# Kernel tuning notes

Measured on AMD Instinct MI355X. Metric: run time of the kernel, lower is better.

Reference implementation:

```python
import jax, jax.numpy as jnp
import numpy as np

N = 20000      # nodes
E = 320000     # directed edges (before self loops)
IN_DIM = 384
D = 256        # hidden_dim
H = 4          # heads
C = D // H     # per-head channels = 64
L = 3          # layers
NEG_SLOPE = 0.2
LN_EPS = 1e-5


def setup_inputs() -> dict:
    key = jax.random.key(0)
    ks = jax.random.split(key, 8)
    return {
        "x": jax.random.normal(ks[0], (N, IN_DIM), jnp.float32),
        "edge_index": jax.random.randint(ks[1], (2, E), 0, N),
        "w_in": jax.random.normal(ks[2], (IN_DIM, D), jnp.float32) * 0.05,
        "b_in": jnp.zeros((D,), jnp.float32),
        "wl": jax.random.normal(ks[3], (L, D, D), jnp.float32) * 0.05,
        "wr": jax.random.normal(ks[4], (L, D, D), jnp.float32) * 0.05,
        "att": jax.random.normal(ks[5], (L, H, C), jnp.float32) * 0.05,
        "bias": jnp.zeros((L, D), jnp.float32),
        "ln_g": jnp.ones((L, D), jnp.float32),
        "ln_b": jnp.zeros((L, D), jnp.float32),
    }


def _layernorm(h, g, b):
    mu = jnp.mean(h, axis=-1, keepdims=True)
    var = jnp.mean(jnp.square(h - mu), axis=-1, keepdims=True)
    return (h - mu) * jax.lax.rsqrt(var + LN_EPS) * g + b


def _gatv2(h, src, dst, Wl, Wr, a, b):
    # PyG GATv2Conv, concat=True, eval mode (no dropout), self-loops already in src/dst.
    xl = (h @ Wl).reshape(N, H, C)   # source transform (lin_l)
    xr = (h @ Wr).reshape(N, H, C)   # target transform (lin_r)
    x_j = xl[src]                    # [E', H, C] gathered source messages
    e = jnp.einsum('ehc,hc->eh', jax.nn.leaky_relu(x_j + xr[dst], NEG_SLOPE), a)
    # segment softmax over edges grouped by destination node
    m = jax.ops.segment_max(e, dst, num_segments=N)
    e = jnp.exp(e - m[dst])
    s = jax.ops.segment_sum(e, dst, num_segments=N)
    alpha = e / (s[dst] + 1e-16)     # [E', H]
    out = jax.ops.segment_sum(x_j * alpha[:, :, None], dst, num_segments=N)
    return out.reshape(N, D) + b


def reference(x, edge_index, w_in, b_in, wl, wr, att, bias, ln_g, ln_b):
    loops = jnp.arange(N, dtype=edge_index.dtype)
    src = jnp.concatenate([edge_index[0], loops])
    dst = jnp.concatenate([edge_index[1], loops])
    h = x @ w_in + b_in
    for l in range(L):
        h_new = _layernorm(_gatv2(h, src, dst, wl[l], wr[l], att[l], bias[l]),
                           ln_g[l], ln_b[l])
        h = h + h_new  # shapes always match since concat output == hidden_dim
    norm = jnp.linalg.norm(h, axis=-1, keepdims=True)
    return h / jnp.maximum(norm, 1e-12)
```

## Files before the change

kernel.cpp:

```cpp
#include <hip/hip_runtime.h>
#include <math.h>

#define N_NODES 20000
#define E_EDGES 320000
#define E_TOT   (E_EDGES + N_NODES)
#define IN_DIM  384
#define DIM     256
#define LAYERS  3
#define NEG_SLOPE 0.2f
#define LN_EPS 1e-5f

typedef unsigned short u16;
typedef unsigned int u32;
typedef __attribute__((ext_vector_type(8))) short short8;
typedef __attribute__((ext_vector_type(8))) __bf16 bf16x8;
typedef __attribute__((ext_vector_type(4))) float f32x4;

__device__ inline u16 f2bf(float f) {
    u32 u = __builtin_bit_cast(u32, f);
    return (u16)((u + 0x7fffu + ((u >> 16) & 1u)) >> 16);
}
__device__ inline float bf2f(u16 s) {
    u32 u = (u32)s << 16;
    return __builtin_bit_cast(float, u);
}

__device__ inline float2 f2add(float2 a, float2 b) { return make_float2(a.x + b.x, a.y + b.y); }
__device__ inline float2 f2mul(float2 a, float2 b) { return make_float2(a.x * b.x, a.y * b.y); }
__device__ inline float2 f2fma(float2 a, float2 b, float2 c) {
    return make_float2(fmaf(a.x, b.x, c.x), fmaf(a.y, b.y, c.y));
}
__device__ inline float2 f2max(float2 a, float2 b) {
    return make_float2(fmaxf(a.x, b.x), fmaxf(a.y, b.y));
}

__device__ inline f32x4 mfma_bf16(short8 a, short8 b, f32x4 c) {
    return __builtin_amdgcn_mfma_f32_16x16x32_bf16(
        __builtin_bit_cast(bf16x8, a), __builtin_bit_cast(bf16x8, b), c, 0, 0, 0);
}

__device__ inline void gl_lds16(const u16* g, u16* l) {
    __builtin_amdgcn_global_load_lds(
        (const __attribute__((address_space(1))) u32*)g,
        (__attribute__((address_space(3))) u32*)l, 16, 0, 0);
}

#define W_IN_ELEMS (IN_DIM * DIM)
#define W_LR_ELEMS (2 * DIM * DIM)
#define W_TOT (W_IN_ELEMS + LAYERS * W_LR_ELEMS)

#define N4X (N_NODES * IN_DIM / 4)
__global__ void prep_kernel(const int* __restrict__ ei, int* __restrict__ counts,
                            const float* __restrict__ x, u16* __restrict__ x_bf,
                            const float* __restrict__ w_in, const float* __restrict__ wl,
                            const float* __restrict__ wr, u16* __restrict__ w_out) {
    int tid = blockIdx.x * 256 + threadIdx.x;
    if (tid < E_TOT) {
        int d = (tid < E_EDGES) ? ei[E_EDGES + tid] : (tid - E_EDGES);
        atomicAdd(&counts[d], 1);
        return;
    }
    tid -= E_TOT;
    if (tid < N4X) {
        float4 v = reinterpret_cast<const float4*>(x)[tid];
        reinterpret_cast<ushort4*>(x_bf)[tid] =
            make_ushort4(f2bf(v.x), f2bf(v.y), f2bf(v.z), f2bf(v.w));
        return;
    }
    tid -= N4X;
    if (tid < W_TOT) {
        float v;
        if (tid < W_IN_ELEMS) {
            int n = tid / IN_DIM, k = tid % IN_DIM;
            v = w_in[k * DIM + n];
        } else {
            int j = tid - W_IN_ELEMS;
            int l = j / W_LR_ELEMS;
            int r = j % W_LR_ELEMS;
            int n = r >> 8, k = r & 255;
            const float* W = (n < DIM) ? wl : wr;
            v = W[l * DIM * DIM + k * DIM + (n & 255)];
        }
        w_out[tid] = f2bf(v);
    }
}

__global__ __launch_bounds__(1024) void scan_kernel(const int* __restrict__ counts,
                                                    int* __restrict__ row_ptr) {
    __shared__ int sums[1024];
    const int t = threadIdx.x;
    const int CH = (N_NODES + 1023) / 1024;
    int base = t * CH;
    int local = 0;
    for (int i = 0; i < CH; ++i) {
        int idx = base + i;
        if (idx < N_NODES) local += counts[idx];
    }
    sums[t] = local;
    __syncthreads();
    for (int off = 1; off < 1024; off <<= 1) {
        int v = (t >= off) ? sums[t - off] : 0;
        __syncthreads();
        sums[t] += v;
        __syncthreads();
    }
    int run = (t == 0) ? 0 : sums[t - 1];
    for (int i = 0; i < CH; ++i) {
        int idx = base + i;
        if (idx < N_NODES) { row_ptr[idx] = run; run += counts[idx]; }
    }
    if (t == 1023) row_ptr[N_NODES] = sums[1023];
}

__global__ void scatter_kernel(const int* __restrict__ ei, const int* __restrict__ row_ptr,
                               int* __restrict__ cursor, int* __restrict__ csr_src) {
    int e = blockIdx.x * 256 + threadIdx.x;
    if (e >= E_TOT) return;
    int s, d;
    if (e < E_EDGES) { s = ei[e]; d = ei[E_EDGES + e]; }
    else { s = e - E_EDGES; d = s; }
    int pos = row_ptr[d] + atomicAdd(&cursor[d], 1);
    csr_src[pos] = s;
}

#define BM 128
#define BN 128
#define BK 64
template <int K, bool BIAS, int NX, int NTOT>
__global__ __launch_bounds__(256) void gemm_mfma(
    const u16* __restrict__ A, const u16* __restrict__ B,
    const float* __restrict__ bias, u16* __restrict__ Cbf,
    int M, int ldc) {
    __shared__ u16 lds[2][2][BM * BK];
    const int tid = threadIdx.x;
    const int w = tid >> 6, lane = tid & 63;
    const int wm = w >> 1, wn = w & 1;

    int lin = blockIdx.y * NX + blockIdx.x;
    constexpr int q8 = NTOT >> 3, r8 = NTOT & 7;
    int k8 = lin & 7, j8 = lin >> 3;
    int bid2 = k8 * q8 + min(k8, r8) + j8;
    const int bm = (bid2 / NX) * BM, bn = (bid2 % NX) * BN;

    const int fr = lane & 15, q = lane >> 4;

    f32x4 acc[4][4] = {};

    const int s_row = tid >> 3, s_blk = tid & 7;
    constexpr int NT = K / BK;

#pragma unroll
    for (int i = 0; i < 4; ++i) {
        int row = i * 32 + s_row;
        int gcol = ((s_blk ^ (row & 7)) << 3);
        int base = (i * 256 + (tid & ~63)) << 3;
        int ra = min(bm + row, M - 1);
        gl_lds16(A + (size_t)ra * K + gcol, &lds[0][0][base]);
        gl_lds16(B + (size_t)(bn + row) * K + gcol, &lds[0][1][base]);
    }
    __syncthreads();

    for (int t = 0; t < NT; ++t) {
        const int p = t & 1;
        if (t + 1 < NT) {
            const int k0 = (t + 1) * BK;
#pragma unroll
            for (int i = 0; i < 4; ++i) {
                int row = i * 32 + s_row;
                int gcol = ((s_blk ^ (row & 7)) << 3);
                int base = (i * 256 + (tid & ~63)) << 3;
                int ra = min(bm + row, M - 1);
                gl_lds16(A + (size_t)ra * K + k0 + gcol, &lds[p ^ 1][0][base]);
                gl_lds16(B + (size_t)(bn + row) * K + k0 + gcol, &lds[p ^ 1][1][base]);
            }
        }
        short8 a_f[2][4], b_f[2][4];
#pragma unroll
        for (int kk = 0; kk < 2; ++kk) {
#pragma unroll
            for (int mi = 0; mi < 4; ++mi) {
                int row = wm * 64 + mi * 16 + fr;
                a_f[kk][mi] = *reinterpret_cast<const short8*>(
                    &lds[p][0][row * BK + ((((kk << 2) + q) ^ (row & 7)) << 3)]);
            }
#pragma unroll
            for (int ni = 0; ni < 4; ++ni) {
                int row = wn * 64 + ni * 16 + fr;
                b_f[kk][ni] = *reinterpret_cast<const short8*>(
                    &lds[p][1][row * BK + ((((kk << 2) + q) ^ (row & 7)) << 3)]);
            }
        }
#pragma unroll
        for (int kk = 0; kk < 2; ++kk)
#pragma unroll
            for (int mi = 0; mi < 4; ++mi)
#pragma unroll
                for (int ni = 0; ni < 4; ++ni)
                    acc[mi][ni] = mfma_bf16(a_f[kk][mi], b_f[kk][ni], acc[mi][ni]);
        __syncthreads();
    }

#pragma unroll
    for (int mi = 0; mi < 4; ++mi) {
#pragma unroll
        for (int r = 0; r < 4; ++r) {
            int row = bm + wm * 64 + mi * 16 + q * 4 + r;
            if (row >= M) continue;
#pragma unroll
            for (int ni = 0; ni < 4; ++ni) {
                int col = bn + wn * 64 + ni * 16 + fr;
                float v = acc[mi][ni][r];
                if (BIAS) v += bias[col];
                Cbf[(size_t)row * ldc + col] = f2bf(v);
            }
        }
    }
}

template <bool LAST>
__global__ __launch_bounds__(256) void gat_edge(const u16* __restrict__ xlr_bf,
                                                const int* __restrict__ row_ptr,
                                                const int* __restrict__ csr_src,
                                                const float* __restrict__ att,
                                                const float* __restrict__ bias,
                                                const float* __restrict__ ln_g,
                                                const float* __restrict__ ln_b,
                                                u16* __restrict__ h_bf,
                                                float* __restrict__ out) {
    const int wave = threadIdx.x >> 6;
    const int lane = threadIdx.x & 63;
    const int node = blockIdx.x * 4 + wave;
    if (node >= N_NODES) return;
    const int c4 = lane << 2;

    const float4 a4 = *reinterpret_cast<const float4*>(att + c4);
    const float2 a01 = make_float2(a4.x, a4.y), a23 = make_float2(a4.z, a4.w);
    const ushort4 uxr = *reinterpret_cast<const ushort4*>(xlr_bf + (size_t)node * 512 + 256 + c4);
    const float2 xr01 = make_float2(bf2f(uxr.x), bf2f(uxr.y));
    const float2 xr23 = make_float2(bf2f(uxr.z), bf2f(uxr.w));
    const float2 k02 = make_float2(NEG_SLOPE, NEG_SLOPE);

    float sA = 0.f, sB = 0.f;
    float2 aA01 = make_float2(0.f, 0.f), aA23 = aA01, aB01 = aA01, aB23 = aA01;

    const int e0 = row_ptr[node];
    const int d = row_ptr[node + 1] - e0;

    for (int base = 0; base < d; base += 64) {
        const int rem = min(d - base, 64);
        const int idx = base + lane;
        const int my_src = (idx < d) ? csr_src[e0 + idx] : node;
        for (int k = 0; k < rem; k += 4) {
            ushort4 uu[4];
#pragma unroll
            for (int j = 0; j < 4; ++j) {
                int s = __shfl(my_src, k + j);
                uu[j] = *reinterpret_cast<const ushort4*>(xlr_bf + (size_t)s * 512 + c4);
            }
#pragma unroll
            for (int j = 0; j < 4; ++j) {
                float2 v01 = make_float2(bf2f(uu[j].x), bf2f(uu[j].y));
                float2 v23 = make_float2(bf2f(uu[j].z), bf2f(uu[j].w));
                float2 t01 = f2add(v01, xr01), t23 = f2add(v23, xr23);
                float2 l01 = f2max(t01, f2mul(t01, k02));
                float2 l23 = f2max(t23, f2mul(t23, k02));
                float2 dd = f2fma(l01, a01, f2mul(l23, a23));
                float p = dd.x + dd.y;
                p += __shfl_xor(p, 1);
                p += __shfl_xor(p, 2);
                p += __shfl_xor(p, 4);
                p += __shfl_xor(p, 8);
                float pe = (k + j < rem) ? __expf(p) : 0.f;
                float2 pe2 = make_float2(pe, pe);
                if (j & 1) {
                    sB += pe;
                    aB01 = f2fma(pe2, v01, aB01);
                    aB23 = f2fma(pe2, v23, aB23);
                } else {
                    sA += pe;
                    aA01 = f2fma(pe2, v01, aA01);
                    aA23 = f2fma(pe2, v23, aA23);
                }
            }
        }
    }

    float s = sA + sB;
    float inv = 1.f / (s + 1e-16f);
    float2 inv2 = make_float2(inv, inv);
    float2 acc01 = f2add(aA01, aB01), acc23 = f2add(aA23, aB23);
    const float4 b4 = *reinterpret_cast<const float4*>(bias + c4);
    float2 o01 = f2fma(acc01, inv2, make_float2(b4.x, b4.y));
    float2 o23 = f2fma(acc23, inv2, make_float2(b4.z, b4.w));

    float lsum = o01.x + o01.y + o23.x + o23.y;
    float lsq = o01.x * o01.x + o01.y * o01.y + o23.x * o23.x + o23.y * o23.y;
#pragma unroll
    for (int off = 1; off < 64; off <<= 1) {
        lsum += __shfl_xor(lsum, off);
        lsq  += __shfl_xor(lsq, off);
    }
    float mu = lsum * (1.f / 256.f);
    float var = lsq * (1.f / 256.f) - mu * mu;
    float rstd = rsqrtf(var + LN_EPS);
    const float4 g4  = *reinterpret_cast<const float4*>(ln_g + c4);
    const float4 lb4 = *reinterpret_cast<const float4*>(ln_b + c4);
    float2 mu2 = make_float2(-mu, -mu), rstd2 = make_float2(rstd, rstd);

    const ushort4 uh = *reinterpret_cast<const ushort4*>(h_bf + (size_t)node * DIM + c4);
    float2 h01 = make_float2(bf2f(uh.x), bf2f(uh.y));
    float2 h23 = make_float2(bf2f(uh.z), bf2f(uh.w));
    float2 n01 = f2fma(f2mul(f2add(o01, mu2), rstd2), make_float2(g4.x, g4.y),
                       make_float2(lb4.x, lb4.y));
    float2 n23 = f2fma(f2mul(f2add(o23, mu2), rstd2), make_float2(g4.z, g4.w),
                       make_float2(lb4.z, lb4.w));
    h01 = f2add(h01, n01);
    h23 = f2add(h23, n23);

    if (LAST) {
        float nsq = h01.x * h01.x + h01.y * h01.y + h23.x * h23.x + h23.y * h23.y;
#pragma unroll
        for (int off = 1; off < 64; off <<= 1) nsq += __shfl_xor(nsq, off);
        float ninv = 1.f / fmaxf(sqrtf(nsq), 1e-12f);
        float4 o = make_float4(h01.x * ninv, h01.y * ninv, h23.x * ninv, h23.y * ninv);
        *reinterpret_cast<float4*>(out + (size_t)node * DIM + c4) = o;
    } else {
        *reinterpret_cast<ushort4*>(h_bf + (size_t)node * DIM + c4) =
            make_ushort4(f2bf(h01.x), f2bf(h01.y), f2bf(h23.x), f2bf(h23.y));
    }
}

extern "C" void kernel_launch(void* const* d_in, const int* in_sizes, int n_in,
                              void* d_out, int out_size, void* d_ws, size_t ws_size,
                              hipStream_t stream) {
    const float* x    = (const float*)d_in[0];
    const int*   ei   = (const int*)d_in[1];
    const float* w_in = (const float*)d_in[2];
    const float* b_in = (const float*)d_in[3];
    const float* wl   = (const float*)d_in[4];
    const float* wr   = (const float*)d_in[5];
    const float* att  = (const float*)d_in[6];
    const float* bias = (const float*)d_in[7];
    const float* ln_g = (const float*)d_in[8];
    const float* ln_b = (const float*)d_in[9];

    char* p = (char*)d_ws;
    u16*   h_bf   = (u16*)p;              p += (size_t)N_NODES * DIM * 2;
    u16*   xlr_bf = (u16*)p;              p += (size_t)N_NODES * 512 * 2;
    u16*   w_bf   = (u16*)p;              p += (size_t)W_TOT * 2;
    int* row_ptr  = (int*)p;              p += (N_NODES + 1) * 4;
    int* counts   = (int*)p;              p += N_NODES * 4;
    int* cursor   = (int*)p;              p += N_NODES * 4;
    int* csr_src  = (int*)p;

    u16* x_bf = xlr_bf;

    hipMemsetAsync(counts, 0, sizeof(int) * 2 * N_NODES, stream);
    {
        int total = E_TOT + N4X + W_TOT;
        prep_kernel<<<(total + 255) / 256, 256, 0, stream>>>(
            ei, counts, x, x_bf, w_in, wl, wr, w_bf);
    }
    scan_kernel<<<1, 1024, 0, stream>>>(counts, row_ptr);
    scatter_kernel<<<(E_TOT + 255) / 256, 256, 0, stream>>>(ei, row_ptr, cursor, csr_src);

    constexpr int NYT = (N_NODES + BM - 1) / BM;
    gemm_mfma<IN_DIM, true, 2, 2 * NYT><<<dim3(2, NYT), 256, 0, stream>>>(
        x_bf, w_bf, b_in, h_bf, N_NODES, DIM);

    for (int l = 0; l < LAYERS; ++l) {
        const u16* wlr = w_bf + W_IN_ELEMS + (size_t)l * W_LR_ELEMS;
        gemm_mfma<DIM, false, 4, 4 * NYT><<<dim3(4, NYT), 256, 0, stream>>>(
            h_bf, wlr, nullptr, xlr_bf, N_NODES, 512);
        if (l < LAYERS - 1) {
            gat_edge<false><<<(N_NODES + 3) / 4, 256, 0, stream>>>(
                xlr_bf, row_ptr, csr_src,
                att + (size_t)l * DIM, bias + (size_t)l * DIM,
                ln_g + (size_t)l * DIM, ln_b + (size_t)l * DIM,
                h_bf, nullptr);
        } else {
            gat_edge<true><<<(N_NODES + 3) / 4, 256, 0, stream>>>(
                xlr_bf, row_ptr, csr_src,
                att + (size_t)l * DIM, bias + (size_t)l * DIM,
                ln_g + (size_t)l * DIM, ln_b + (size_t)l * DIM,
                h_bf, (float*)d_out);
        }
    }
}
```

Before: 260.1 us.

## Shrink GEMM tiles, software-pipeline edge gathers, use DPP reductions

The GEMM tile drops from 128x128 to 64x64, which quadruples the block count to fill more compute units, and the grid dimensions are updated to match. The edge-aggregation loop is rewritten to keep three 4-edge groups of source-feature loads in flight, reading csr_src directly per edge instead of through a lane shuffle, so gather latency overlaps with compute. The 16-lane head reductions now use DPP row ops instead of shfl_xor, and the residual h load is hoisted to the start of the kernel. Smaller tiles reduce data reuse per block, and the triple buffering raises register pressure.

```diff
diff --git a/kernel.cpp b/kernel.cpp
--- a/kernel.cpp
+++ b/kernel.cpp
@@ -32,6 +32,26 @@
 }
 __device__ inline float2 f2max(float2 a, float2 b) {
     return make_float2(fmaxf(a.x, b.x), fmaxf(a.y, b.y));
+}
+
+template <int CTRL>
+__device__ inline float dpp_add(float v) {
+    int x = __builtin_bit_cast(int, v);
+    int y = __builtin_amdgcn_update_dpp(0, x, CTRL, 0xF, 0xF, true);
+    return v + __builtin_bit_cast(float, y);
+}
+__device__ inline float red16(float p) {
+    p = dpp_add<0xB1>(p);
+    p = dpp_add<0x4E>(p);
+    p = dpp_add<0x141>(p);
+    p = dpp_add<0x140>(p);
+    return p;
+}
+__device__ inline float red64(float v) {
+    v = red16(v);
+    v += __shfl_xor(v, 16);
+    v += __shfl_xor(v, 32);
+    return v;
 }
 
 __device__ inline f32x4 mfma_bf16(short8 a, short8 b, f32x4 c) {
@@ -123,8 +143,8 @@
     csr_src[pos] = s;
 }
 
-#define BM 128
-#define BN 128
+#define BM 64
+#define BN 64
 #define BK 64
 template <int K, bool BIAS, int NX, int NTOT>
 __global__ __launch_bounds__(256) void gemm_mfma(
@@ -143,14 +163,13 @@
     const int bm = (bid2 / NX) * BM, bn = (bid2 % NX) * BN;
 
     const int fr = lane & 15, q = lane >> 4;
-
-    f32x4 acc[4][4] = {};
+    f32x4 acc[2][2] = {};
 
     const int s_row = tid >> 3, s_blk = tid & 7;
     constexpr int NT = K / BK;
 
 #pragma unroll
-    for (int i = 0; i < 4; ++i) {
+    for (int i = 0; i < 2; ++i) {
         int row = i * 32 + s_row;
         int gcol = ((s_blk ^ (row & 7)) << 3);
         int base = (i * 256 + (tid & ~63)) << 3;
@@ -165,7 +184,7 @@
         if (t + 1 < NT) {
             const int k0 = (t + 1) * BK;
 #pragma unroll
-            for (int i = 0; i < 4; ++i) {
+            for (int i = 0; i < 2; ++i) {
                 int row = i * 32 + s_row;
                 int gcol = ((s_blk ^ (row & 7)) << 3);
                 int base = (i * 256 + (tid & ~63)) << 3;
@@ -174,41 +193,39 @@
                 gl_lds16(B + (size_t)(bn + row) * K + k0 + gcol, &lds[p ^ 1][1][base]);
             }
         }
-        short8 a_f[2][4], b_f[2][4];
 #pragma unroll
         for (int kk = 0; kk < 2; ++kk) {
-#pragma unroll
-            for (int mi = 0; mi < 4; ++mi) {
-                int row = wm * 64 + mi * 16 + fr;
-                a_f[kk][mi] = *reinterpret_cast<const short8*>(
+            short8 a_f[2], b_f[2];
+#pragma unroll
+            for (int mi = 0; mi < 2; ++mi) {
+                int row = wm * 32 + mi * 16 + fr;
+                a_f[mi] = *reinterpret_cast<const short8*>(
                     &lds[p][0][row * BK + ((((kk << 2) + q) ^ (row & 7)) << 3)]);
             }
 #pragma unroll
-            for (int ni = 0; ni < 4; ++ni) {
-                int row = wn * 64 + ni * 16 + fr;
-                b_f[kk][ni] = *reinterpret_cast<const short8*>(
+            for (int ni = 0; ni < 2; ++ni) {
+                int row = wn * 32 + ni * 16 + fr;
+                b_f[ni] = *reinterpret_cast<const short8*>(
                     &lds[p][1][row * BK + ((((kk << 2) + q) ^ (row & 7)) << 3)]);
             }
+#pragma unroll
+            for (int mi = 0; mi < 2; ++mi)
+#pragma unroll
+                for (int ni = 0; ni < 2; ++ni)
+                    acc[mi][ni] = mfma_bf16(a_f[mi], b_f[ni], acc[mi][ni]);
         }
-#pragma unroll
-        for (int kk = 0; kk < 2; ++kk)
-#pragma unroll
-            for (int mi = 0; mi < 4; ++mi)
-#pragma unroll
-                for (int ni = 0; ni < 4; ++ni)
-                    acc[mi][ni] = mfma_bf16(a_f[kk][mi], b_f[kk][ni], acc[mi][ni]);
         __syncthreads();
     }
 
 #pragma unroll
-    for (int mi = 0; mi < 4; ++mi) {
+    for (int mi = 0; mi < 2; ++mi) {
 #pragma unroll
         for (int r = 0; r < 4; ++r) {
-            int row = bm + wm * 64 + mi * 16 + q * 4 + r;
+            int row = bm + wm * 32 + mi * 16 + q * 4 + r;
             if (row >= M) continue;
 #pragma unroll
-            for (int ni = 0; ni < 4; ++ni) {
-                int col = bn + wn * 64 + ni * 16 + fr;
+            for (int ni = 0; ni < 2; ++ni) {
+                int col = bn + wn * 32 + ni * 16 + fr;
                 float v = acc[mi][ni][r];
                 if (BIAS) v += bias[col];
                 Cbf[(size_t)row * ldc + col] = f2bf(v);
@@ -236,6 +253,7 @@
     const float4 a4 = *reinterpret_cast<const float4*>(att + c4);
     const float2 a01 = make_float2(a4.x, a4.y), a23 = make_float2(a4.z, a4.w);
     const ushort4 uxr = *reinterpret_cast<const ushort4*>(xlr_bf + (size_t)node * 512 + 256 + c4);
+    const ushort4 uh  = *reinterpret_cast<const ushort4*>(h_bf + (size_t)node * DIM + c4);
     const float2 xr01 = make_float2(bf2f(uxr.x), bf2f(uxr.y));
     const float2 xr23 = make_float2(bf2f(uxr.z), bf2f(uxr.w));
     const float2 k02 = make_float2(NEG_SLOPE, NEG_SLOPE);
@@ -246,44 +264,56 @@
     const int e0 = row_ptr[node];
     const int d = row_ptr[node + 1] - e0;
 
-    for (int base = 0; base < d; base += 64) {
-        const int rem = min(d - base, 64);
-        const int idx = base + lane;
-        const int my_src = (idx < d) ? csr_src[e0 + idx] : node;
-        for (int k = 0; k < rem; k += 4) {
-            ushort4 uu[4];
-#pragma unroll
-            for (int j = 0; j < 4; ++j) {
-                int s = __shfl(my_src, k + j);
-                uu[j] = *reinterpret_cast<const ushort4*>(xlr_bf + (size_t)s * 512 + c4);
-            }
-#pragma unroll
-            for (int j = 0; j < 4; ++j) {
-                float2 v01 = make_float2(bf2f(uu[j].x), bf2f(uu[j].y));
-                float2 v23 = make_float2(bf2f(uu[j].z), bf2f(uu[j].w));
-                float2 t01 = f2add(v01, xr01), t23 = f2add(v23, xr23);
-                float2 l01 = f2max(t01, f2mul(t01, k02));
-                float2 l23 = f2max(t23, f2mul(t23, k02));
-                float2 dd = f2fma(l01, a01, f2mul(l23, a23));
-                float p = dd.x + dd.y;
-                p += __shfl_xor(p, 1);
-                p += __shfl_xor(p, 2);
-                p += __shfl_xor(p, 4);
-                p += __shfl_xor(p, 8);
-                float pe = (k + j < rem) ? __expf(p) : 0.f;
-                float2 pe2 = make_float2(pe, pe);
-                if (j & 1) {
-                    sB += pe;
-                    aB01 = f2fma(pe2, v01, aB01);
-                    aB23 = f2fma(pe2, v23, aB23);
-                } else {
-                    sA += pe;
-                    aA01 = f2fma(pe2, v01, aA01);
-                    aA23 = f2fma(pe2, v23, aA23);
-                }
-            }
-        }
-    }
+    ushort4 bA[4], bB[4], bC[4];
+
+#define ISSUE(buf, baseidx)                                                        \
+    {                                                                              \
+        _Pragma("unroll")                                                          \
+        for (int j = 0; j < 4; ++j) {                                              \
+            int idx = (baseidx) + j;                                               \
+            int s = (idx < d) ? csr_src[e0 + idx] : node;                          \
+            buf[j] = *reinterpret_cast<const ushort4*>(xlr_bf + (size_t)s * 512 + c4); \
+        }                                                                          \
+    }
+
+#define PROC(buf, baseidx)                                                         \
+    {                                                                              \
+        _Pragma("unroll")                                                          \
+        for (int j = 0; j < 4; ++j) {                                              \
+            float2 v01 = make_float2(bf2f(buf[j].x), bf2f(buf[j].y));              \
+            float2 v23 = make_float2(bf2f(buf[j].z), bf2f(buf[j].w));              \
+            float2 t01 = f2add(v01, xr01), t23 = f2add(v23, xr23);                 \
+            float2 l01 = f2max(t01, f2mul(t01, k02));                              \
+            float2 l23 = f2max(t23, f2mul(t23, k02));                              \
+            float2 dd = f2fma(l01, a01, f2mul(l23, a23));                          \
+            float p = red16(dd.x + dd.y);                                          \
+            float pe = ((baseidx) + j < d) ? __expf(p) : 0.f;                      \
+            float2 pe2 = make_float2(pe, pe);                                      \
+            if (j & 1) {                                                           \
+                sB += pe;                                                          \
+                aB01 = f2fma(pe2, v01, aB01);                                      \
+                aB23 = f2fma(pe2, v23, aB23);                                      \
+            } else {                                                               \
+                sA += pe;                                                          \
+                aA01 = f2fma(pe2, v01, aA01);                                      \
+                aA23 = f2fma(pe2, v23, aA23);                                      \
+            }                                                                      \
+        }                                                                          \
+    }
+
+    ISSUE(bA, 0);
+    ISSUE(bB, 4);
+    ISSUE(bC, 8);
+    for (int base = 0; base < d; base += 12) {
+        PROC(bA, base);
+        if (base + 12 < d) ISSUE(bA, base + 12);
+        PROC(bB, base + 4);
+        if (base + 16 < d) ISSUE(bB, base + 16);
+        PROC(bC, base + 8);
+        if (base + 20 < d) ISSUE(bC, base + 20);
+    }
+#undef ISSUE
+#undef PROC
 
     float s = sA + sB;
     float inv = 1.f / (s + 1e-16f);
@@ -293,13 +323,8 @@
     float2 o01 = f2fma(acc01, inv2, make_float2(b4.x, b4.y));
     float2 o23 = f2fma(acc23, inv2, make_float2(b4.z, b4.w));
 
-    float lsum = o01.x + o01.y + o23.x + o23.y;
-    float lsq = o01.x * o01.x + o01.y * o01.y + o23.x * o23.x + o23.y * o23.y;
-#pragma unroll
-    for (int off = 1; off < 64; off <<= 1) {
-        lsum += __shfl_xor(lsum, off);
-        lsq  += __shfl_xor(lsq, off);
-    }
+    float lsum = red64(o01.x + o01.y + o23.x + o23.y);
+    float lsq  = red64(o01.x * o01.x + o01.y * o01.y + o23.x * o23.x + o23.y * o23.y);
     float mu = lsum * (1.f / 256.f);
     float var = lsq * (1.f / 256.f) - mu * mu;
     float rstd = rsqrtf(var + LN_EPS);
@@ -307,7 +332,6 @@
     const float4 lb4 = *reinterpret_cast<const float4*>(ln_b + c4);
     float2 mu2 = make_float2(-mu, -mu), rstd2 = make_float2(rstd, rstd);
 
-    const ushort4 uh = *reinterpret_cast<const ushort4*>(h_bf + (size_t)node * DIM + c4);
     float2 h01 = make_float2(bf2f(uh.x), bf2f(uh.y));
     float2 h23 = make_float2(bf2f(uh.z), bf2f(uh.w));
     float2 n01 = f2fma(f2mul(f2add(o01, mu2), rstd2), make_float2(g4.x, g4.y),
@@ -318,9 +342,7 @@
     h23 = f2add(h23, n23);
 
     if (LAST) {
-        float nsq = h01.x * h01.x + h01.y * h01.y + h23.x * h23.x + h23.y * h23.y;
-#pragma unroll
-        for (int off = 1; off < 64; off <<= 1) nsq += __shfl_xor(nsq, off);
+        float nsq = red64(h01.x * h01.x + h01.y * h01.y + h23.x * h23.x + h23.y * h23.y);
         float ninv = 1.f / fmaxf(sqrtf(nsq), 1e-12f);
         float4 o = make_float4(h01.x * ninv, h01.y * ninv, h23.x * ninv, h23.y * ninv);
         *reinterpret_cast<float4*>(out + (size_t)node * DIM + c4) = o;
@@ -365,12 +387,12 @@
     scatter_kernel<<<(E_TOT + 255) / 256, 256, 0, stream>>>(ei, row_ptr, cursor, csr_src);
 
     constexpr int NYT = (N_NODES + BM - 1) / BM;
-    gemm_mfma<IN_DIM, true, 2, 2 * NYT><<<dim3(2, NYT), 256, 0, stream>>>(
+    gemm_mfma<IN_DIM, true, 4, 4 * NYT><<<dim3(4, NYT), 256, 0, stream>>>(
         x_bf, w_bf, b_in, h_bf, N_NODES, DIM);
 
     for (int l = 0; l < LAYERS; ++l) {
         const u16* wlr = w_bf + W_IN_ELEMS + (size_t)l * W_LR_ELEMS;
-        gemm_mfma<DIM, false, 4, 4 * NYT><<<dim3(4, NYT), 256, 0, stream>>>(
+        gemm_mfma<DIM, false, 8, 8 * NYT><<<dim3(8, NYT), 256, 0, stream>>>(
             h_bf, wlr, nullptr, xlr_bf, N_NODES, 512);
         if (l < LAYERS - 1) {
             gat_edge<false><<<(N_NODES + 3) / 4, 256, 0, stream>>>(
```

Result: slower. 349.6 us (+34.4%).
